# Performance work log

Hardware: AMD Instinct MI355X
Metric: run time of the kernel (lower is better)

Reference implementation:

```python
import jax, jax.numpy as jnp
import numpy as np

N_NODES = 100000
BN_EPS = 1e-5


def _linear_params(key, fan_in, fan_out):
    k1, k2 = jax.random.split(key)
    lim = 1.0 / np.sqrt(fan_in)
    W = jax.random.uniform(k1, (fan_in, fan_out), jnp.float32, -lim, lim)
    b = jax.random.uniform(k2, (fan_out,), jnp.float32, -lim, lim)
    return W, b


def setup_inputs() -> dict:
    key = jax.random.key(0)
    ks = jax.random.split(key, 24)
    in_ch, hid, tdim, L = 17, 64, 32, 2
    E = 1600000
    inp = {}
    inp["x"] = jax.random.normal(ks[0], (N_NODES, in_ch), jnp.float32)
    inp["edge_index"] = jax.random.randint(ks[1], (2, E), 0, N_NODES, jnp.int64)
    inp["edge_dts"] = jax.random.uniform(ks[2], (E,), jnp.float32) * 100.0
    inp["batch_size"] = 10000
    # TimeEncode params (learned, TGAT init)
    inp["basis_freq"] = jnp.asarray(1.0 / 10 ** np.linspace(0, 9, tdim), jnp.float32)
    inp["phase"] = jnp.zeros((tdim,), jnp.float32)
    # TMP edge MLP: in = 2*in_ch + tdim
    mi = 2 * in_ch + tdim
    inp["tmp_W1"], inp["tmp_b1"] = _linear_params(ks[3], mi, mi // 2)
    inp["tmp_W2"], inp["tmp_b2"] = _linear_params(ks[4], mi // 2, in_ch)
    inp["proj_W"], inp["proj_b"] = _linear_params(ks[5], in_ch, hid)
    # SMP layers (stacked over L)
    si = 2 * hid
    W1s, b1s, W2s, b2s = [], [], [], []
    for l in range(L):
        W1, b1 = _linear_params(ks[6 + 2 * l], si, si // 2)
        W2, b2 = _linear_params(ks[7 + 2 * l], si // 2, hid)
        W1s.append(W1); b1s.append(b1); W2s.append(W2); b2s.append(b2)
    inp["smp_W1"] = jnp.stack(W1s); inp["smp_b1"] = jnp.stack(b1s)
    inp["smp_W2"] = jnp.stack(W2s); inp["smp_b2"] = jnp.stack(b2s)
    inp["bn_gamma"] = jnp.ones((L, hid), jnp.float32)
    inp["bn_beta"] = jnp.zeros((L, hid), jnp.float32)
    # classifier head
    inp["clf_W1"], inp["clf_b1"] = _linear_params(ks[12], hid, hid)
    inp["clf_g1"] = jnp.ones((hid,), jnp.float32); inp["clf_bb1"] = jnp.zeros((hid,), jnp.float32)
    inp["clf_W2"], inp["clf_b2"] = _linear_params(ks[13], hid, hid // 2)
    inp["clf_g2"] = jnp.ones((hid // 2,), jnp.float32); inp["clf_bb2"] = jnp.zeros((hid // 2,), jnp.float32)
    inp["clf_W3"], inp["clf_b3"] = _linear_params(ks[14], hid // 2, 1)
    return inp


def _segment_mean(vals, idx, n):
    s = jax.ops.segment_sum(vals, idx, num_segments=n)
    c = jax.ops.segment_sum(jnp.ones((idx.shape[0], 1), vals.dtype), idx, num_segments=n)
    return s / jnp.maximum(c, 1.0)


def _bn(x, g, b):
    m = x.mean(0)
    v = x.var(0)
    return (x - m) * jax.lax.rsqrt(v + BN_EPS) * g + b


def reference(x, edge_index, edge_dts, batch_size, basis_freq, phase,
              tmp_W1, tmp_b1, tmp_W2, tmp_b2, proj_W, proj_b,
              smp_W1, smp_b1, smp_W2, smp_b2, bn_gamma, bn_beta,
              clf_W1, clf_b1, clf_g1, clf_bb1,
              clf_W2, clf_b2, clf_g2, clf_bb2, clf_W3, clf_b3):
    src, dst = edge_index[0], edge_index[1]  # x_j = x[src], x_i = x[dst]
    n = x.shape[0]
    # TimeEncode: cos(t * freq + phase)  -> [E, time_dim]
    rel = jnp.cos(edge_dts[:, None] * basis_freq + phase)
    # --- TMP conv (applied once) ---
    x_i = x[dst]
    m_in = jnp.concatenate([x_i, x[src], rel], axis=-1)
    p = jnp.tanh(jax.nn.relu(m_in @ tmp_W1 + tmp_b1) @ tmp_W2 + tmp_b2)
    msg = (2.0 * p - 1.0) * x_i  # (p - q) * x_i with q = 1 - p
    h = x + _segment_mean(msg, dst, n)
    # --- project to hidden ---
    h = h @ proj_W + proj_b
    # --- L SMP layers with BatchNorm + ReLU (dropout = eval/identity) ---
    L = smp_W1.shape[0]
    for l in range(L):
        h_i = h[dst]
        m_in = jnp.concatenate([h_i, h[src]], axis=-1)
        p = jnp.tanh(jax.nn.relu(m_in @ smp_W1[l] + smp_b1[l]) @ smp_W2[l] + smp_b2[l])
        h = h + _segment_mean((2.0 * p - 1.0) * h_i, dst, n)
        h = jax.nn.relu(_bn(h, bn_gamma[l], bn_beta[l]))
    # --- classifier on seed nodes ---
    z = h[:batch_size]
    z = jax.nn.relu(_bn(z @ clf_W1 + clf_b1, clf_g1, clf_bb1))
    z = jax.nn.relu(_bn(z @ clf_W2 + clf_b2, clf_g2, clf_bb2))
    return z @ clf_W3 + clf_b3  # [batch_size, 1] logits
```

## Files before the change

### kernel.cpp

```cpp
#include <hip/hip_runtime.h>
#include <hip/hip_bf16.h>


typedef float  f32x4 __attribute__((ext_vector_type(4)));
typedef short  s16x8 __attribute__((ext_vector_type(8)));

__device__ __forceinline__ float tanh_factor(float u) {
  float e = __expf(2.0f * u);
  return 1.0f - 4.0f / (e + 1.0f);
}

__device__ __forceinline__ void atomic_add_f32(float* p, float v) {
  unsafeAtomicAdd(p, v);
}

__device__ __forceinline__ unsigned short f2bf(float f) {
  __hip_bfloat16 b = __float2bfloat16(f);
  return *(unsigned short*)&b;
}
__device__ __forceinline__ float bf2f(unsigned short u) {
  unsigned int v = ((unsigned int)u) << 16;
  return *(float*)&v;
}

__global__ __launch_bounds__(256) void k_hist(
    const int* __restrict__ ei, int* __restrict__ cntI, int E)
{
  int e = blockIdx.x * 256 + threadIdx.x;
  if (e < E) atomicAdd(&cntI[ei[E + e]], 1);
}

__global__ __launch_bounds__(256) void k_scan_block(
    const int* __restrict__ cntI, int* __restrict__ cursor,
    int* __restrict__ bsum, int N)
{
  __shared__ int s[256];
  const int t = threadIdx.x;
  int i = blockIdx.x * 256 + t;
  int v = (i < N) ? cntI[i] : 0;
  s[t] = v;
  for (int off = 1; off < 256; off <<= 1) {
    __syncthreads();
    int x = (t >= off) ? s[t - off] : 0;
    __syncthreads();
    s[t] += x;
  }
  __syncthreads();
  if (i < N) cursor[i] = s[t] - v;
  if (t == 255) bsum[blockIdx.x] = s[255];
}

__global__ __launch_bounds__(512) void k_scan_bsum(int* __restrict__ bsum, int nb)
{
  __shared__ int s[512];
  const int t = threadIdx.x;
  int v = (t < nb) ? bsum[t] : 0;
  s[t] = v;
  for (int off = 1; off < 512; off <<= 1) {
    __syncthreads();
    int x = (t >= off) ? s[t - off] : 0;
    __syncthreads();
    s[t] += x;
  }
  __syncthreads();
  if (t < nb) bsum[t] = s[t] - v;
}

__global__ __launch_bounds__(256) void k_scan_add(
    int* __restrict__ cursor, const int* __restrict__ bsum, int N)
{
  int i = blockIdx.x * 256 + threadIdx.x;
  if (i < N) cursor[i] += bsum[blockIdx.x];
}

__global__ __launch_bounds__(256) void k_scatter(
    const int* __restrict__ ei, const float* __restrict__ dts,
    int* __restrict__ cursor, int2* __restrict__ pairS,
    float* __restrict__ dtsS, int E)
{
  int e = blockIdx.x * 256 + threadIdx.x;
  if (e >= E) return;
  int d = ei[E + e];
  int pos = atomicAdd(&cursor[d], 1);
  pairS[pos] = make_int2(d, ei[e]);
  dtsS[pos] = dts[e];
}

__global__ __launch_bounds__(256) void prep1(
    const float* __restrict__ x, const float* __restrict__ tW1,
    const float* __restrict__ tW2, unsigned short* __restrict__ xb,
    unsigned short* __restrict__ W1t1, unsigned short* __restrict__ W2t1, int N)
{
  int i = blockIdx.x * 256 + threadIdx.x;
  int totalX = N * 24;
  for (int idx = i; idx < totalX; idx += gridDim.x * 256) {
    int n = idx / 24, c = idx - n * 24;
    xb[idx] = (c < 17) ? f2bf(x[n * 17 + c]) : (unsigned short)0;
  }
  if (i < 48 * 96) {
    int n = i / 96, k = i - n * 96;
    int src = (k < 17) ? k : (k >= 24 && k < 41) ? (k - 24 + 17)
            : (k >= 48 && k < 80) ? (k - 48 + 34) : -1;
    W1t1[i] = (n < 33 && src >= 0) ? f2bf(tW1[src * 33 + n]) : (unsigned short)0;
  }
  if (i < 32 * 64) {
    int n = i / 64, k = i - n * 64;
    W2t1[i] = (n < 17 && k < 33) ? f2bf(tW2[k * 17 + n]) : (unsigned short)0;
  }
}

__global__ __launch_bounds__(256, 3) void phase1_edge_mfma(
    const unsigned short* __restrict__ xb, const int2* __restrict__ pairS,
    const float* __restrict__ dtsS, const float* __restrict__ freq,
    const float* __restrict__ phs,
    const unsigned short* __restrict__ W1t1, const float* __restrict__ b1,
    const unsigned short* __restrict__ W2t1, const float* __restrict__ b2,
    float* __restrict__ accum, int E, int ntiles)
{
  __shared__ unsigned short sA[64][104];
  __shared__ unsigned short sHid[64][72];
  __shared__ float sRed[64][20];
  __shared__ int   sDst[64];

  const int t = threadIdx.x;
  const int wv = t >> 6, lane = t & 63, l16 = lane & 15, quad = lane >> 4;

  s16x8 w1f[3][3], w2f[2][2];
  float bias1[3], bias2[2];
#pragma unroll
  for (int cb = 0; cb < 3; cb++) {
    int n = cb * 16 + l16;
#pragma unroll
    for (int kb = 0; kb < 3; kb++)
      w1f[cb][kb] = *(const s16x8*)&W1t1[n * 96 + kb * 32 + quad * 8];
    bias1[cb] = (n < 33) ? b1[n] : 0.0f;
  }
#pragma unroll
  for (int cb = 0; cb < 2; cb++) {
    int n = cb * 16 + l16;
#pragma unroll
    for (int kb = 0; kb < 2; kb++)
      w2f[cb][kb] = *(const s16x8*)&W2t1[n * 64 + kb * 32 + quad * 8];
    bias2[cb] = (n < 17) ? b2[n] : 0.0f;
  }

  for (int i = t; i < 64 * 28; i += 256) {
    int r = i / 28, c = i - r * 28;
    int col = (c < 6) ? 18 + c : (c < 12) ? 42 + (c - 6) : 80 + (c - 12);
    sA[r][col] = 0;
  }
  for (int i = t; i < 64 * 16; i += 256) {
    int r = i >> 4, c = 48 + (i & 15);
    sHid[r][c] = 0;
  }

  for (int tile = blockIdx.x; tile < ntiles; tile += gridDim.x) {
    const int eb = tile << 6;

    {
      int e_l = t >> 2, q = t & 3;
      int er = eb + e_l; if (er >= E) er = E - 1;
      if (q < 2) {
        int2 p = pairS[er];
        int node = q ? p.y : p.x;
        if (!q) sDst[e_l] = p.x;
        const unsigned short* src = &xb[(size_t)node * 24];
        int base = q ? 24 : 0;
        *(uint4*)&sA[e_l][base]     = *(const uint4*)&src[0];
        *(uint4*)&sA[e_l][base + 8] = *(const uint4*)&src[8];
        *(unsigned int*)&sA[e_l][base + 16] = *(const unsigned int*)&src[16];
      } else {
        float dt = dtsS[er];
        int k0 = (q == 2) ? 0 : 16;
        unsigned short tmp[16] __attribute__((aligned(16)));
#pragma unroll
        for (int j = 0; j < 16; j++)
          tmp[j] = f2bf(__cosf(fmaf(dt, freq[k0 + j], phs[k0 + j])));
        *(uint4*)&sA[e_l][48 + k0]     = *(const uint4*)&tmp[0];
        *(uint4*)&sA[e_l][48 + k0 + 8] = *(const uint4*)&tmp[8];
      }
    }
    __syncthreads();

    f32x4 a1[3];
#pragma unroll
    for (int cb = 0; cb < 3; cb++)
      a1[cb] = (f32x4){bias1[cb], bias1[cb], bias1[cb], bias1[cb]};
#pragma unroll
    for (int kb = 0; kb < 3; kb++) {
      s16x8 aF = *(const s16x8*)&sA[wv * 16 + l16][kb * 32 + quad * 8];
#pragma unroll
      for (int cb = 0; cb < 3; cb++)
        a1[cb] = __builtin_amdgcn_mfma_f32_16x16x32_bf16(aF, w1f[cb][kb], a1[cb], 0, 0, 0);
    }
#pragma unroll
    for (int cb = 0; cb < 3; cb++)
#pragma unroll
      for (int reg = 0; reg < 4; reg++)
        sHid[wv * 16 + quad * 4 + reg][cb * 16 + l16] = f2bf(fmaxf(a1[cb][reg], 0.0f));
    __syncthreads();

    f32x4 a2[2];
#pragma unroll
    for (int cb = 0; cb < 2; cb++)
      a2[cb] = (f32x4){bias2[cb], bias2[cb], bias2[cb], bias2[cb]};
#pragma unroll
    for (int kb = 0; kb < 2; kb++) {
      s16x8 aF = *(const s16x8*)&sHid[wv * 16 + l16][kb * 32 + quad * 8];
#pragma unroll
      for (int cb = 0; cb < 2; cb++)
        a2[cb] = __builtin_amdgcn_mfma_f32_16x16x32_bf16(aF, w2f[cb][kb], a2[cb], 0, 0, 0);
    }

#pragma unroll
    for (int reg = 0; reg < 4; reg++) {
      int row = wv * 16 + quad * 4 + reg;
      bool ok = (eb + row < E);
      sRed[row][l16] = ok ? tanh_factor(a2[0][reg]) : 0.0f;
      if (l16 == 0) sRed[row][16] = ok ? tanh_factor(a2[1][reg]) : 0.0f;
    }
    __syncthreads();

    if (t < 68) {
      int col = t % 17;
      int r0 = (t / 17) * 16;
      float run = 0.0f;
      int cur = sDst[r0];
#pragma unroll
      for (int k = 0; k < 16; k++) {
        int r = r0 + k;
        int d = sDst[r];
        float v = sRed[r][col];
        if (d != cur) {
          atomic_add_f32(&accum[(size_t)cur * 17 + col], run);
          run = 0.0f; cur = d;
        }
        run += v;
      }
      atomic_add_f32(&accum[(size_t)cur * 17 + col], run);
    }
    __syncthreads();
  }
}

__global__ __launch_bounds__(256) void phase1_node(
    const float* __restrict__ x, const float* __restrict__ acc1,
    const int* __restrict__ cntI, const float* __restrict__ Wp,
    const float* __restrict__ bp, float* __restrict__ h, int N)
{
  __shared__ float s0[4][20];
  const int t = threadIdx.x;
  const int nb = blockIdx.x << 2;
  if (t < 68) {
    int nl = t / 17, c = t % 17;
    int n = nb + nl;
    float v = 0.0f;
    if (n < N) {
      float cnt = fmaxf((float)cntI[n], 1.0f);
      v = x[n * 17 + c] * (1.0f + acc1[n * 17 + c] / cnt);
    }
    s0[nl][c] = v;
  }
  __syncthreads();
  int nl = t >> 6, j = t & 63;
  int n = nb + nl;
  if (n < N) {
    float acc = bp[j];
#pragma unroll
    for (int c = 0; c < 17; c++) acc = fmaf(s0[nl][c], Wp[c * 64 + j], acc);
    h[n * 64 + j] = acc;
  }
}

__global__ __launch_bounds__(256) void prep_w(
    const float* __restrict__ sW1, const float* __restrict__ sW2,
    unsigned short* __restrict__ W1t, unsigned short* __restrict__ W2t)
{
  int i = blockIdx.x * 256 + threadIdx.x;
  if (i < 2 * 64 * 128) {
    int l = i >> 13; int r = i & 8191; int n = r >> 7; int k = r & 127;
    W1t[i] = f2bf(sW1[((size_t)l * 128 + k) * 64 + n]);
  }
  if (i < 2 * 64 * 64) {
    int l = i >> 12; int r = i & 4095; int n = r >> 6; int k = r & 63;
    W2t[i] = f2bf(sW2[((size_t)l * 64 + k) * 64 + n]);
  }
}

__global__ void prep_P(
    const float* __restrict__ h, const unsigned short* __restrict__ W1t,
    const float* __restrict__ b1, unsigned short* __restrict__ P1,
    unsigned short* __restrict__ P2, int N)
{
  __shared__ unsigned short sH[64][72];
  const int t = threadIdx.x;
  const int wv = t >> 6, lane = t & 63, l16 = lane & 15, quad = lane >> 4;
  const int nb = blockIdx.x << 6;

#pragma unroll
  for (int i = 0; i < 4; i++) {
    int g = t + i * 256;
    int r = g >> 4, c4 = (g & 15) << 2;
    int n = nb + r; if (n >= N) n = N - 1;
    float4 v = *(const float4*)&h[(size_t)n * 64 + c4];
    ushort4 o = { f2bf(v.x), f2bf(v.y), f2bf(v.z), f2bf(v.w) };
    *(ushort4*)&sH[r][c4] = o;
  }
  __syncthreads();

  const int n = nb + wv * 16 + l16;
#pragma unroll
  for (int half = 0; half < 2; half++) {
    f32x4 acc[4];
#pragma unroll
    for (int cb = 0; cb < 4; cb++) {
      if (half == 0) {
        float4 bv = *(const float4*)&b1[cb * 16 + quad * 4];
        acc[cb] = (f32x4){bv.x, bv.y, bv.z, bv.w};
      } else {
        acc[cb] = (f32x4){0.0f, 0.0f, 0.0f, 0.0f};
      }
    }
#pragma unroll
    for (int kb = 0; kb < 2; kb++) {
      s16x8 bF = *(const s16x8*)&sH[wv * 16 + l16][kb * 32 + quad * 8];
#pragma unroll
      for (int cb = 0; cb < 4; cb++) {
        s16x8 aF = *(const s16x8*)&W1t[(cb * 16 + l16) * 128 + half * 64 + kb * 32 + quad * 8];
        acc[cb] = __builtin_amdgcn_mfma_f32_16x16x32_bf16(aF, bF, acc[cb], 0, 0, 0);
      }
    }
    if (n < N) {
      unsigned short* P = half ? P2 : P1;
#pragma unroll
      for (int cb = 0; cb < 4; cb++) {
        ushort4 o = { f2bf(acc[cb][0]), f2bf(acc[cb][1]),
                      f2bf(acc[cb][2]), f2bf(acc[cb][3]) };
        *(ushort4*)&P[(size_t)n * 64 + cb * 16 + quad * 4] = o;
      }
    }
  }
}

__global__ __launch_bounds__(256, 4) void phase2_edge(
    const unsigned short* __restrict__ P1, const unsigned short* __restrict__ P2,
    const int2* __restrict__ pairS,
    const unsigned short* __restrict__ W2t, const float* __restrict__ b2,
    float* __restrict__ accum, int E, int ntiles)
{
  __shared__ unsigned short sA[64][136];
  __shared__ int sDst[64];
  float* sRedF = (float*)&sA[0][0];

  const int t = threadIdx.x;
  const int wv = t >> 6, lane = t & 63, l16 = lane & 15, quad = lane >> 4;

  s16x8 w2f[4][2];
  f32x4 bias2v[4];
#pragma unroll
  for (int cb = 0; cb < 4; cb++) {
#pragma unroll
    for (int kb = 0; kb < 2; kb++)
      w2f[cb][kb] = *(const s16x8*)&W2t[(cb * 16 + l16) * 64 + kb * 32 + quad * 8];
    float4 bv = *(const float4*)&b2[cb * 16 + quad * 4];
    bias2v[cb] = (f32x4){bv.x, bv.y, bv.z, bv.w};
  }

  const int eRow = wv * 16 + l16;

  for (int tile = blockIdx.x; tile < ntiles; tile += gridDim.x) {
    const int eb = tile << 6;

#pragma unroll
    for (int i = 0; i < 4; i++) {
      int g = t + i * 256; int r = g >> 4, c = g & 15;
      int er = eb + r; if (er >= E) er = E - 1;
      int2 p = pairS[er];
      int node = (c >= 8) ? p.y : p.x;
      if (c == 0) sDst[r] = p.x;
      const unsigned short* src = (c >= 8) ? P2 : P1;
      *(uint4*)&sA[r][c * 8] = *(const uint4*)&src[(size_t)node * 64 + (c & 7) * 8];
    }
    __syncthreads();

    s16x8 hidf[2];
#pragma unroll
    for (int kb = 0; kb < 2; kb++) {
      s16x8 x1 = *(const s16x8*)&sA[eRow][kb * 32 + quad * 8];
      s16x8 x2 = *(const s16x8*)&sA[eRow][64 + kb * 32 + quad * 8];
      s16x8 hf;
#pragma unroll
      for (int j = 0; j < 8; j++) {
        float a = bf2f((unsigned short)x1[j]);
        float b = bf2f((unsigned short)x2[j]);
        hf[j] = (short)f2bf(fmaxf(a + b, 0.0f));
      }
      hidf[kb] = hf;
    }

    f32x4 acc[4];
#pragma unroll
    for (int cb = 0; cb < 4; cb++) acc[cb] = bias2v[cb];
#pragma unroll
    for (int kb = 0; kb < 2; kb++)
#pragma unroll
      for (int cb = 0; cb < 4; cb++)
        acc[cb] = __builtin_amdgcn_mfma_f32_16x16x32_bf16(w2f[cb][kb], hidf[kb], acc[cb], 0, 0, 0);

    bool ok = (eb + eRow < E);
#pragma unroll
    for (int cb = 0; cb < 4; cb++) {
      f32x4 f;
#pragma unroll
      for (int reg = 0; reg < 4; reg++)
        f[reg] = ok ? tanh_factor(acc[cb][reg]) : 0.0f;
      *(f32x4*)&sRedF[eRow * 68 + cb * 16 + quad * 4] = f;
    }

    {
      int j = lane;
      int r0 = wv * 16;
      float run = 0.0f;
      int cur = sDst[r0];
#pragma unroll
      for (int k = 0; k < 16; k++) {
        int r = r0 + k;
        int d = sDst[r];
        float v = sRedF[r * 68 + j];
        if (d != cur) {
          atomic_add_f32(&accum[(size_t)cur * 64 + j], run);
          run = 0.0f; cur = d;
        }
        run += v;
      }
      atomic_add_f32(&accum[(size_t)cur * 64 + j], run);
    }
    __syncthreads();
  }
}

__global__ __launch_bounds__(256) void node_update_bn(
    float* __restrict__ h, const float* __restrict__ accum,
    const int* __restrict__ cntI, float* __restrict__ bns,
    float* __restrict__ bnq, int N)
{
  const int t = threadIdx.x;
  float ls = 0.0f, lq = 0.0f;
  int total = N * 64;
  for (int idx = blockIdx.x * 256 + t; idx < total; idx += gridDim.x * 256) {
    int n = idx >> 6;
    float cnt = fmaxf((float)cntI[n], 1.0f);
    float v = h[idx] * (1.0f + accum[idx] / cnt);
    h[idx] = v;
    ls += v; lq += v * v;
  }
  __shared__ float ss[256], sq[256];
  ss[t] = ls; sq[t] = lq;
  __syncthreads();
  if (t < 64) {
    float s = ss[t] + ss[t + 64] + ss[t + 128] + ss[t + 192];
    float q = sq[t] + sq[t + 64] + sq[t + 128] + sq[t + 192];
    atomic_add_f32(&bns[t], s);
    atomic_add_f32(&bnq[t], q);
  }
}

__global__ __launch_bounds__(256) void bn_apply_relu(
    float* __restrict__ d, const float* __restrict__ bns,
    const float* __restrict__ bnq, const float* __restrict__ gam,
    const float* __restrict__ bet, int total, int cmask, float invRows)
{
  for (int idx = blockIdx.x * 256 + threadIdx.x; idx < total;
       idx += gridDim.x * 256) {
    int c = idx & cmask;
    float m = bns[c] * invRows;
    float var = bnq[c] * invRows - m * m;
    float sc = gam[c] * rsqrtf(var + 1e-5f);
    d[idx] = fmaxf((d[idx] - m) * sc + bet[c], 0.0f);
  }
}

__global__ __launch_bounds__(256) void clf_mm_bn(
    const float* __restrict__ in, const float* __restrict__ W,
    const float* __restrict__ b, float* __restrict__ out,
    float* __restrict__ bns, float* __restrict__ bnq,
    int rows, int K, int cshift)
{
  const int t = threadIdx.x;
  const int C = 1 << cshift;
  int total = rows << cshift;
  float ls = 0.0f, lq = 0.0f;
  for (int idx = blockIdx.x * 256 + t; idx < total; idx += gridDim.x * 256) {
    int n = idx >> cshift;
    int c = idx & (C - 1);
    float acc = b[c];
#pragma unroll 8
    for (int k = 0; k < K; k++) acc = fmaf(in[n * K + k], W[(k << cshift) + c], acc);
    out[idx] = acc;
    ls += acc; lq += acc * acc;
  }
  __shared__ float ss[256], sq[256];
  ss[t] = ls; sq[t] = lq;
  __syncthreads();
  if (t < C) {
    float s = 0.0f, q = 0.0f;
    for (int i = t; i < 256; i += C) { s += ss[i]; q += sq[i]; }
    atomic_add_f32(&bns[t], s);
    atomic_add_f32(&bnq[t], q);
  }
}

__global__ __launch_bounds__(256) void clf_final(
    const float* __restrict__ z2, const float* __restrict__ W3,
    const float* __restrict__ b3, float* __restrict__ out, int rows)
{
  int n = blockIdx.x * 256 + threadIdx.x;
  if (n >= rows) return;
  float acc = b3[0];
#pragma unroll
  for (int k = 0; k < 32; k++) acc = fmaf(z2[n * 32 + k], W3[k], acc);
  out[n] = acc;
}

extern "C" void kernel_launch(void* const* d_in, const int* in_sizes, int n_in,
                              void* d_out, int out_size, void* d_ws, size_t ws_size,
                              hipStream_t stream)
{
  const float* x    = (const float*)d_in[0];
  const int*   ei   = (const int*)  d_in[1];
  const float* dts  = (const float*)d_in[2];
  const float* freq = (const float*)d_in[4];
  const float* phs  = (const float*)d_in[5];
  const float* tW1  = (const float*)d_in[6];
  const float* tb1  = (const float*)d_in[7];
  const float* tW2  = (const float*)d_in[8];
  const float* tb2  = (const float*)d_in[9];
  const float* pW   = (const float*)d_in[10];
  const float* pb   = (const float*)d_in[11];
  const float* sW1  = (const float*)d_in[12];
  const float* sb1  = (const float*)d_in[13];
  const float* sW2  = (const float*)d_in[14];
  const float* sb2  = (const float*)d_in[15];
  const float* bng  = (const float*)d_in[16];
  const float* bnb  = (const float*)d_in[17];
  const float* cW1  = (const float*)d_in[18];
  const float* cb1  = (const float*)d_in[19];
  const float* cg1  = (const float*)d_in[20];
  const float* cbb1 = (const float*)d_in[21];
  const float* cW2  = (const float*)d_in[22];
  const float* cb2  = (const float*)d_in[23];
  const float* cg2  = (const float*)d_in[24];
  const float* cbb2 = (const float*)d_in[25];
  const float* cW3  = (const float*)d_in[26];
  const float* cb3  = (const float*)d_in[27];
  float* out = (float*)d_out;

  const int N = in_sizes[0] / 17;
  const int E = in_sizes[1] / 2;
  const int B = out_size;

  float* ws     = (float*)d_ws;
  float* h      = ws;
  float* acc2   = h    + (size_t)N * 64;
  float* acc1   = acc2 + (size_t)N * 64;
  float* z1     = acc1;
  float* z2     = z1 + (size_t)B * 64;
  float* bns    = acc1 + (size_t)N * 17;
  float* bnq    = bns + 64;
  unsigned short* W1t = (unsigned short*)(bnq + 64);
  unsigned short* W2t = W1t + 2 * 64 * 128;
  int*   cntI   = (int*)(W2t + 2 * 64 * 64);
  int*   cursor = cntI + N;
  int*   bsum   = cursor + N;
  int2*  pairS  = (int2*)(bsum + 512);
  float* dtsS   = (float*)(pairS + (size_t)E);
  unsigned short* xb = (unsigned short*)(dtsS + (size_t)E);
  unsigned short* P1 = (unsigned short*)dtsS;
  size_t r1a = (size_t)E + ((size_t)N * 24 + 1) / 2;
  size_t r1b = ((size_t)N * 64 + 1) / 2;
  size_t r1  = r1a > r1b ? r1a : r1b;
  unsigned short* P2   = (unsigned short*)(dtsS + r1);
  unsigned short* W1t1 = P2 + (size_t)N * 64;
  unsigned short* W2t1 = W1t1 + 48 * 96;
  size_t needed = (size_t)((char*)(W2t1 + 32 * 64) - (char*)d_ws);
  if (ws_size < needed) return;

  const int ntiles = (E + 63) / 64;
  const int NB = (N + 255) / 256;
  if (NB > 512) return;

  hipMemsetAsync(cntI, 0, (size_t)N * 4, stream);
  hipMemsetAsync(acc1, 0, (size_t)N * 17 * 4, stream);
  k_hist<<<(E + 255) / 256, 256, 0, stream>>>(ei, cntI, E);
  k_scan_block<<<NB, 256, 0, stream>>>(cntI, cursor, bsum, N);
  k_scan_bsum<<<1, 512, 0, stream>>>(bsum, NB);
  k_scan_add<<<NB, 256, 0, stream>>>(cursor, bsum, N);
  k_scatter<<<(E + 255) / 256, 256, 0, stream>>>(ei, dts, cursor, pairS, dtsS, E);
  prep_w<<<64, 256, 0, stream>>>(sW1, sW2, W1t, W2t);
  prep1<<<(N * 24 + 255) / 256, 256, 0, stream>>>(x, tW1, tW2, xb, W1t1, W2t1, N);

  phase1_edge_mfma<<<1024, 256, 0, stream>>>(
      xb, pairS, dtsS, freq, phs, W1t1, tb1, W2t1, tb2, acc1, E, ntiles);
  phase1_node<<<(N + 3) / 4, 256, 0, stream>>>(x, acc1, cntI, pW, pb, h, N);

  for (int l = 0; l < 2; l++) {
    prep_P<<<(N + 63) / 64, 256, 0, stream>>>(
        h, W1t + (size_t)l * 64 * 128, sb1 + l * 64, P1, P2, N);
    hipMemsetAsync(acc2, 0, (size_t)N * 64 * 4, stream);
    hipMemsetAsync(bns, 0, 128 * 4, stream);
    phase2_edge<<<1024, 256, 0, stream>>>(
        P1, P2, pairS, W2t + (size_t)l * 64 * 64, sb2 + l * 64, acc2, E, ntiles);
    node_update_bn<<<1024, 256, 0, stream>>>(h, acc2, cntI, bns, bnq, N);
    bn_apply_relu<<<2048, 256, 0, stream>>>(
        h, bns, bnq, bng + l * 64, bnb + l * 64, N * 64, 63, 1.0f / (float)N);
  }

  hipMemsetAsync(bns, 0, 128 * 4, stream);
  clf_mm_bn<<<2500, 256, 0, stream>>>(h, cW1, cb1, z1, bns, bnq, B, 64, 6);
  bn_apply_relu<<<1024, 256, 0, stream>>>(z1, bns, bnq, cg1, cbb1,
                                          B * 64, 63, 1.0f / (float)B);
  hipMemsetAsync(bns, 0, 128 * 4, stream);
  clf_mm_bn<<<1250, 256, 0, stream>>>(z1, cW2, cb2, z2, bns, bnq, B, 64, 5);
  bn_apply_relu<<<512, 256, 0, stream>>>(z2, bns, bnq, cg2, cbb2,
                                         B * 32, 31, 1.0f / (float)B);
  clf_final<<<(B + 255) / 256, 256, 0, stream>>>(z2, cW3, cb3, out, B);
}
```

Before: 908.2 us.

## Make edge kernels wave-independent and split CSR arrays into dst and src+dt

Both edge kernels now hand each wavefront its own 16-edge tile, so every block-level barrier in the tile loop goes away and the four waves in a block no longer lock-step. The sorted edge data is restructured: a new expand kernel writes a per-edge dst array straight from the CSR offsets, and scatter packs src and dt into one int2. This replaces the old pair array plus a separate dt array. The workspace layout is rebuilt around one shared union region, and the phase-1 grid shrinks to 768 blocks. The changes add an extra launch and a serial per-node loop in k_expand.

```diff
diff --git a/kernel.cpp b/kernel.cpp
--- a/kernel.cpp
+++ b/kernel.cpp
@@ -73,17 +73,25 @@
   if (i < N) cursor[i] += bsum[blockIdx.x];
 }
 
+__global__ __launch_bounds__(256) void k_expand(
+    const int* __restrict__ cursor, const int* __restrict__ cntI,
+    int* __restrict__ dstS, int N)
+{
+  int n = blockIdx.x * 256 + threadIdx.x;
+  if (n >= N) return;
+  int s = cursor[n], c = cntI[n];
+  for (int i = 0; i < c; i++) dstS[s + i] = n;
+}
+
 __global__ __launch_bounds__(256) void k_scatter(
     const int* __restrict__ ei, const float* __restrict__ dts,
-    int* __restrict__ cursor, int2* __restrict__ pairS,
-    float* __restrict__ dtsS, int E)
+    int* __restrict__ cursor, int2* __restrict__ srcdtS, int E)
 {
   int e = blockIdx.x * 256 + threadIdx.x;
   if (e >= E) return;
   int d = ei[E + e];
   int pos = atomicAdd(&cursor[d], 1);
-  pairS[pos] = make_int2(d, ei[e]);
-  dtsS[pos] = dts[e];
+  srcdtS[pos] = make_int2(ei[e], __float_as_int(dts[e]));
 }
 
 __global__ __launch_bounds__(256) void prep1(
@@ -110,12 +118,12 @@
 }
 
 __global__ __launch_bounds__(256, 3) void phase1_edge_mfma(
-    const unsigned short* __restrict__ xb, const int2* __restrict__ pairS,
-    const float* __restrict__ dtsS, const float* __restrict__ freq,
+    const unsigned short* __restrict__ xb, const int* __restrict__ dstS,
+    const int2* __restrict__ srcdtS, const float* __restrict__ freq,
     const float* __restrict__ phs,
     const unsigned short* __restrict__ W1t1, const float* __restrict__ b1,
     const unsigned short* __restrict__ W2t1, const float* __restrict__ b2,
-    float* __restrict__ accum, int E, int ntiles)
+    float* __restrict__ accum, int E, int nwt)
 {
   __shared__ unsigned short sA[64][104];
   __shared__ unsigned short sHid[64][72];
@@ -124,6 +132,7 @@
 
   const int t = threadIdx.x;
   const int wv = t >> 6, lane = t & 63, l16 = lane & 15, quad = lane >> 4;
+  const int r0 = wv * 16;
 
   s16x8 w1f[3][3], w2f[2][2];
   float bias1[3], bias2[2];
@@ -144,43 +153,43 @@
     bias2[cb] = (n < 17) ? b2[n] : 0.0f;
   }
 
-  for (int i = t; i < 64 * 28; i += 256) {
-    int r = i / 28, c = i - r * 28;
+  for (int i = lane; i < 16 * 28; i += 64) {
+    int rr = r0 + i / 28, c = i % 28;
     int col = (c < 6) ? 18 + c : (c < 12) ? 42 + (c - 6) : 80 + (c - 12);
-    sA[r][col] = 0;
-  }
-  for (int i = t; i < 64 * 16; i += 256) {
-    int r = i >> 4, c = 48 + (i & 15);
-    sHid[r][c] = 0;
-  }
-
-  for (int tile = blockIdx.x; tile < ntiles; tile += gridDim.x) {
-    const int eb = tile << 6;
+    sA[rr][col] = 0;
+  }
+  for (int i = lane; i < 256; i += 64)
+    sHid[r0 + (i >> 4)][48 + (i & 15)] = 0;
+
+  const int gw = blockIdx.x * 4 + wv;
+  const int nw = gridDim.x * 4;
+
+  for (int tile = gw; tile < nwt; tile += nw) {
+    const int eb = tile << 4;
 
     {
-      int e_l = t >> 2, q = t & 3;
-      int er = eb + e_l; if (er >= E) er = E - 1;
+      int e_loc = lane >> 2, q = lane & 3;
+      int rr = r0 + e_loc;
+      int er = eb + e_loc; if (er >= E) er = E - 1;
       if (q < 2) {
-        int2 p = pairS[er];
-        int node = q ? p.y : p.x;
-        if (!q) sDst[e_l] = p.x;
+        int node = q ? srcdtS[er].x : dstS[er];
+        if (!q) sDst[rr] = node;
         const unsigned short* src = &xb[(size_t)node * 24];
         int base = q ? 24 : 0;
-        *(uint4*)&sA[e_l][base]     = *(const uint4*)&src[0];
-        *(uint4*)&sA[e_l][base + 8] = *(const uint4*)&src[8];
-        *(unsigned int*)&sA[e_l][base + 16] = *(const unsigned int*)&src[16];
+        *(uint4*)&sA[rr][base]     = *(const uint4*)&src[0];
+        *(uint4*)&sA[rr][base + 8] = *(const uint4*)&src[8];
+        *(unsigned int*)&sA[rr][base + 16] = *(const unsigned int*)&src[16];
       } else {
-        float dt = dtsS[er];
+        float dt = __int_as_float(srcdtS[er].y);
         int k0 = (q == 2) ? 0 : 16;
         unsigned short tmp[16] __attribute__((aligned(16)));
 #pragma unroll
         for (int j = 0; j < 16; j++)
           tmp[j] = f2bf(__cosf(fmaf(dt, freq[k0 + j], phs[k0 + j])));
-        *(uint4*)&sA[e_l][48 + k0]     = *(const uint4*)&tmp[0];
-        *(uint4*)&sA[e_l][48 + k0 + 8] = *(const uint4*)&tmp[8];
+        *(uint4*)&sA[rr][48 + k0]     = *(const uint4*)&tmp[0];
+        *(uint4*)&sA[rr][48 + k0 + 8] = *(const uint4*)&tmp[8];
       }
     }
-    __syncthreads();
 
     f32x4 a1[3];
 #pragma unroll
@@ -188,7 +197,7 @@
       a1[cb] = (f32x4){bias1[cb], bias1[cb], bias1[cb], bias1[cb]};
 #pragma unroll
     for (int kb = 0; kb < 3; kb++) {
-      s16x8 aF = *(const s16x8*)&sA[wv * 16 + l16][kb * 32 + quad * 8];
+      s16x8 aF = *(const s16x8*)&sA[r0 + l16][kb * 32 + quad * 8];
 #pragma unroll
       for (int cb = 0; cb < 3; cb++)
         a1[cb] = __builtin_amdgcn_mfma_f32_16x16x32_bf16(aF, w1f[cb][kb], a1[cb], 0, 0, 0);
@@ -197,8 +206,7 @@
     for (int cb = 0; cb < 3; cb++)
 #pragma unroll
       for (int reg = 0; reg < 4; reg++)
-        sHid[wv * 16 + quad * 4 + reg][cb * 16 + l16] = f2bf(fmaxf(a1[cb][reg], 0.0f));
-    __syncthreads();
+        sHid[r0 + quad * 4 + reg][cb * 16 + l16] = f2bf(fmaxf(a1[cb][reg], 0.0f));
 
     f32x4 a2[2];
 #pragma unroll
@@ -206,7 +214,7 @@
       a2[cb] = (f32x4){bias2[cb], bias2[cb], bias2[cb], bias2[cb]};
 #pragma unroll
     for (int kb = 0; kb < 2; kb++) {
-      s16x8 aF = *(const s16x8*)&sHid[wv * 16 + l16][kb * 32 + quad * 8];
+      s16x8 aF = *(const s16x8*)&sHid[r0 + l16][kb * 32 + quad * 8];
 #pragma unroll
       for (int cb = 0; cb < 2; cb++)
         a2[cb] = __builtin_amdgcn_mfma_f32_16x16x32_bf16(aF, w2f[cb][kb], a2[cb], 0, 0, 0);
@@ -214,23 +222,20 @@
 
 #pragma unroll
     for (int reg = 0; reg < 4; reg++) {
-      int row = wv * 16 + quad * 4 + reg;
-      bool ok = (eb + row < E);
+      int row = r0 + quad * 4 + reg;
+      bool ok = (eb + quad * 4 + reg < E);
       sRed[row][l16] = ok ? tanh_factor(a2[0][reg]) : 0.0f;
       if (l16 == 0) sRed[row][16] = ok ? tanh_factor(a2[1][reg]) : 0.0f;
     }
-    __syncthreads();
-
-    if (t < 68) {
-      int col = t % 17;
-      int r0 = (t / 17) * 16;
+
+    if (lane < 17) {
+      int col = lane;
       float run = 0.0f;
       int cur = sDst[r0];
 #pragma unroll
       for (int k = 0; k < 16; k++) {
-        int r = r0 + k;
-        int d = sDst[r];
-        float v = sRed[r][col];
+        int d = sDst[r0 + k];
+        float v = sRed[r0 + k][col];
         if (d != cur) {
           atomic_add_f32(&accum[(size_t)cur * 17 + col], run);
           run = 0.0f; cur = d;
@@ -239,7 +244,6 @@
       }
       atomic_add_f32(&accum[(size_t)cur * 17 + col], run);
     }
-    __syncthreads();
   }
 }
 
@@ -344,9 +348,9 @@
 
 __global__ __launch_bounds__(256, 4) void phase2_edge(
     const unsigned short* __restrict__ P1, const unsigned short* __restrict__ P2,
-    const int2* __restrict__ pairS,
+    const int* __restrict__ dstS, const int2* __restrict__ srcdtS,
     const unsigned short* __restrict__ W2t, const float* __restrict__ b2,
-    float* __restrict__ accum, int E, int ntiles)
+    float* __restrict__ accum, int E, int nwt)
 {
   __shared__ unsigned short sA[64][136];
   __shared__ int sDst[64];
@@ -354,6 +358,7 @@
 
   const int t = threadIdx.x;
   const int wv = t >> 6, lane = t & 63, l16 = lane & 15, quad = lane >> 4;
+  const int r0 = wv * 16;
 
   s16x8 w2f[4][2];
   f32x4 bias2v[4];
@@ -366,22 +371,26 @@
     bias2v[cb] = (f32x4){bv.x, bv.y, bv.z, bv.w};
   }
 
-  const int eRow = wv * 16 + l16;
-
-  for (int tile = blockIdx.x; tile < ntiles; tile += gridDim.x) {
-    const int eb = tile << 6;
-
-#pragma unroll
-    for (int i = 0; i < 4; i++) {
-      int g = t + i * 256; int r = g >> 4, c = g & 15;
-      int er = eb + r; if (er >= E) er = E - 1;
-      int2 p = pairS[er];
-      int node = (c >= 8) ? p.y : p.x;
-      if (c == 0) sDst[r] = p.x;
-      const unsigned short* src = (c >= 8) ? P2 : P1;
-      *(uint4*)&sA[r][c * 8] = *(const uint4*)&src[(size_t)node * 64 + (c & 7) * 8];
-    }
-    __syncthreads();
+  const int gw = blockIdx.x * 4 + wv;
+  const int nw = gridDim.x * 4;
+  const int eRow = r0 + l16;
+
+  for (int tile = gw; tile < nwt; tile += nw) {
+    const int eb = tile << 4;
+
+    {
+      int e_loc = lane >> 2, q = lane & 3;
+      int rr = r0 + e_loc;
+      int er = eb + e_loc; if (er >= E) er = E - 1;
+      int node;
+      if (q < 2) { node = dstS[er]; if (!q) sDst[rr] = node; }
+      else       node = srcdtS[er].x;
+      const unsigned short* src = (q < 2 ? P1 : P2) + (size_t)node * 64 + (q & 1) * 32;
+      int cb0 = q * 32;
+#pragma unroll
+      for (int j = 0; j < 4; j++)
+        *(uint4*)&sA[rr][cb0 + j * 8] = *(const uint4*)&src[j * 8];
+    }
 
     s16x8 hidf[2];
 #pragma unroll
@@ -407,7 +416,7 @@
       for (int cb = 0; cb < 4; cb++)
         acc[cb] = __builtin_amdgcn_mfma_f32_16x16x32_bf16(w2f[cb][kb], hidf[kb], acc[cb], 0, 0, 0);
 
-    bool ok = (eb + eRow < E);
+    bool ok = (eb + l16 < E);
 #pragma unroll
     for (int cb = 0; cb < 4; cb++) {
       f32x4 f;
@@ -418,24 +427,20 @@
     }
 
     {
-      int j = lane;
-      int r0 = wv * 16;
       float run = 0.0f;
       int cur = sDst[r0];
 #pragma unroll
       for (int k = 0; k < 16; k++) {
-        int r = r0 + k;
-        int d = sDst[r];
-        float v = sRedF[r * 68 + j];
+        int d = sDst[r0 + k];
+        float v = sRedF[(r0 + k) * 68 + lane];
         if (d != cur) {
-          atomic_add_f32(&accum[(size_t)cur * 64 + j], run);
+          atomic_add_f32(&accum[(size_t)cur * 64 + lane], run);
           run = 0.0f; cur = d;
         }
         run += v;
       }
-      atomic_add_f32(&accum[(size_t)cur * 64 + j], run);
-    }
-    __syncthreads();
+      atomic_add_f32(&accum[(size_t)cur * 64 + lane], run);
+    }
   }
 }
 
@@ -559,33 +564,34 @@
   const int E = in_sizes[1] / 2;
   const int B = out_size;
 
-  float* ws     = (float*)d_ws;
-  float* h      = ws;
-  float* acc2   = h    + (size_t)N * 64;
-  float* acc1   = acc2 + (size_t)N * 64;
-  float* z1     = acc1;
-  float* z2     = z1 + (size_t)B * 64;
-  float* bns    = acc1 + (size_t)N * 17;
-  float* bnq    = bns + 64;
-  unsigned short* W1t = (unsigned short*)(bnq + 64);
-  unsigned short* W2t = W1t + 2 * 64 * 128;
-  int*   cntI   = (int*)(W2t + 2 * 64 * 64);
-  int*   cursor = cntI + N;
-  int*   bsum   = cursor + N;
-  int2*  pairS  = (int2*)(bsum + 512);
-  float* dtsS   = (float*)(pairS + (size_t)E);
-  unsigned short* xb = (unsigned short*)(dtsS + (size_t)E);
-  unsigned short* P1 = (unsigned short*)dtsS;
-  size_t r1a = (size_t)E + ((size_t)N * 24 + 1) / 2;
-  size_t r1b = ((size_t)N * 64 + 1) / 2;
-  size_t r1  = r1a > r1b ? r1a : r1b;
-  unsigned short* P2   = (unsigned short*)(dtsS + r1);
-  unsigned short* W1t1 = P2 + (size_t)N * 64;
+  char* base = (char*)d_ws;
+  size_t off = 0;
+  float* h    = (float*)(base + off); off += (size_t)N * 64 * 4;
+  float* acc2 = (float*)(base + off); off += (size_t)N * 64 * 4;
+  char*  uni  = base + off;           off += (size_t)N * 64 * 4;
+  float* bns  = (float*)(base + off); off += 64 * 4;
+  float* bnq  = (float*)(base + off); off += 64 * 4;
+  unsigned short* W1t = (unsigned short*)(base + off); off += 2 * 64 * 128 * 2;
+  unsigned short* W2t = (unsigned short*)(base + off); off += 2 * 64 * 64 * 2;
+  int* cntI   = (int*)(base + off); off += (size_t)N * 4;
+  int* cursor = (int*)(base + off); off += (size_t)N * 4;
+  int* bsum   = (int*)(base + off); off += 512 * 4;
+  int* dstS   = (int*)(base + off); off += (size_t)E * 4;
+  off = (off + 15) & ~(size_t)15;
+  int2* srcdtS = (int2*)(base + off); off += (size_t)E * 8;
+  size_t needed = off;
+  if (ws_size < needed) return;
+
+  float* acc1 = (float*)uni;
+  unsigned short* xb   = (unsigned short*)(uni + (size_t)N * 17 * 4);
+  unsigned short* W1t1 = xb + (size_t)N * 24;
   unsigned short* W2t1 = W1t1 + 48 * 96;
-  size_t needed = (size_t)((char*)(W2t1 + 32 * 64) - (char*)d_ws);
-  if (ws_size < needed) return;
-
-  const int ntiles = (E + 63) / 64;
+  unsigned short* P1 = (unsigned short*)uni;
+  unsigned short* P2 = P1 + (size_t)N * 64;
+  float* z1 = (float*)uni;
+  float* z2 = z1 + (size_t)B * 64;
+
+  const int nwt = (E + 15) / 16;
   const int NB = (N + 255) / 256;
   if (NB > 512) return;
 
@@ -595,12 +601,13 @@
   k_scan_block<<<NB, 256, 0, stream>>>(cntI, cursor, bsum, N);
   k_scan_bsum<<<1, 512, 0, stream>>>(bsum, NB);
   k_scan_add<<<NB, 256, 0, stream>>>(cursor, bsum, N);
-  k_scatter<<<(E + 255) / 256, 256, 0, stream>>>(ei, dts, cursor, pairS, dtsS, E);
+  k_expand<<<NB, 256, 0, stream>>>(cursor, cntI, dstS, N);
+  k_scatter<<<(E + 255) / 256, 256, 0, stream>>>(ei, dts, cursor, srcdtS, E);
   prep_w<<<64, 256, 0, stream>>>(sW1, sW2, W1t, W2t);
   prep1<<<(N * 24 + 255) / 256, 256, 0, stream>>>(x, tW1, tW2, xb, W1t1, W2t1, N);
 
-  phase1_edge_mfma<<<1024, 256, 0, stream>>>(
-      xb, pairS, dtsS, freq, phs, W1t1, tb1, W2t1, tb2, acc1, E, ntiles);
+  phase1_edge_mfma<<<768, 256, 0, stream>>>(
+      xb, dstS, srcdtS, freq, phs, W1t1, tb1, W2t1, tb2, acc1, E, nwt);
   phase1_node<<<(N + 3) / 4, 256, 0, stream>>>(x, acc1, cntI, pW, pb, h, N);
 
   for (int l = 0; l < 2; l++) {
@@ -609,7 +616,8 @@
     hipMemsetAsync(acc2, 0, (size_t)N * 64 * 4, stream);
     hipMemsetAsync(bns, 0, 128 * 4, stream);
     phase2_edge<<<1024, 256, 0, stream>>>(
-        P1, P2, pairS, W2t + (size_t)l * 64 * 64, sb2 + l * 64, acc2, E, ntiles);
+        P1, P2, dstS, srcdtS, W2t + (size_t)l * 64 * 64, sb2 + l * 64,
+        acc2, E, nwt);
     node_update_bn<<<1024, 256, 0, stream>>>(h, acc2, cntI, bns, bnq, N);
     bn_apply_relu<<<2048, 256, 0, stream>>>(
         h, bns, bnq, bng + l * 64, bnb + l * 64, N * 64, 63, 1.0f / (float)N);
```

Result: no change. 894.3 us (-1.5%).
